# Performance work log

Measured on AMD Instinct MI355X. Metric: run time of the kernel, lower is better.

## Reference

```python
import jax, jax.numpy as jnp
import numpy as np

N_EMBD = 768
N_HEAD = 8
HEAD_DIM = N_EMBD // N_HEAD


def setup_inputs() -> dict:
    key = jax.random.key(0)
    k1, k2, k3 = jax.random.split(key, 3)
    B, T, C = 8, 1024, N_EMBD
    x = jax.random.normal(k1, (B, T, C), dtype=jnp.float32)
    # nn.Linear(C, 3C, bias=False): store as [C, 3C] so y = x @ W
    W_attn = jax.random.normal(k2, (C, 3 * C), dtype=jnp.float32) * (1.0 / np.sqrt(C))
    W_proj = jax.random.normal(k3, (C, C), dtype=jnp.float32) * (1.0 / np.sqrt(C))
    return {"x": x, "W_attn": W_attn, "W_proj": W_proj}


def reference(x, W_attn, W_proj):
    B, T, C = x.shape
    qkv = x @ W_attn                      # [B,T,3C]
    q, k, v = jnp.split(qkv, 3, axis=2)
    # [B,T,C] -> [B,H,T,D]
    def heads(t):
        return t.reshape(B, T, N_HEAD, HEAD_DIM).transpose(0, 2, 1, 3)
    q, k, v = heads(q), heads(k), heads(v)
    scale = 1.0 / np.sqrt(HEAD_DIM)
    att = jnp.einsum('bhtd,bhsd->bhts', q, k) * scale  # [B,H,T,T]
    causal = jnp.tril(jnp.ones((T, T), dtype=bool))
    att = jnp.where(causal[None, None], att, -jnp.inf)
    att = jax.nn.softmax(att, axis=-1)
    y = jnp.einsum('bhts,bhsd->bhtd', att, v)          # [B,H,T,D]
    y = y.transpose(0, 2, 1, 3).reshape(B, T, C)
    return y @ W_proj
```

## Files before the change

kernel.cpp:

```cpp
#include <hip/hip_runtime.h>
#include <stdint.h>

#define Bz 8
#define Tz 1024
#define Cz 768
#define Hz 8
#define Dz 96
#define BHz 64
#define Kz 768

typedef __bf16 bf16x8 __attribute__((ext_vector_type(8)));
typedef unsigned short u16x8 __attribute__((ext_vector_type(8)));
typedef float f32x4 __attribute__((ext_vector_type(4)));

__device__ __forceinline__ unsigned short f2bf(float f) {
  union { float f; unsigned int u; } v; v.f = f;
  unsigned int u = v.u;
  return (unsigned short)((u + 0x7fffu + ((u >> 16) & 1u)) >> 16);
}

__device__ __forceinline__ unsigned int cvtpk(float a, float b) {
  unsigned int r;
  asm("v_cvt_pk_bf16_f32 %0, %1, %2" : "=v"(r) : "v"(a), "v"(b));
  return r;
}

#if defined(__has_builtin)
#if __has_builtin(__builtin_amdgcn_exp2f)
#define EXP2(x) __builtin_amdgcn_exp2f(x)
#endif
#endif
#ifndef EXP2
#define EXP2(x) __expf((x) * 0.6931471805599453f)
#endif

typedef const __attribute__((address_space(1))) void* gas_ptr;
typedef __attribute__((address_space(3))) void* las_ptr;
__device__ __forceinline__ void gl16(const void* g, void* l) {
  __builtin_amdgcn_global_load_lds((gas_ptr)g, (las_ptr)l, 16, 0, 0);
}

__global__ __launch_bounds__(256) void cast_f32_bf16(const float* __restrict__ in,
                                                     unsigned short* __restrict__ out) {
  int i = (blockIdx.x * 256 + threadIdx.x) * 4;
  float4 v = *(const float4*)(in + i);
  union { unsigned short s[4]; uint2 u; } o;
  o.s[0] = f2bf(v.x); o.s[1] = f2bf(v.y); o.s[2] = f2bf(v.z); o.s[3] = f2bf(v.w);
  *(uint2*)(out + i) = o.u;
}

__global__ __launch_bounds__(256) void transpose_cast(const float* __restrict__ in,
                                                      unsigned short* __restrict__ out,
                                                      int R, int Cc) {
  __shared__ unsigned short t[64][72];
  int bx = blockIdx.x * 64;
  int by = blockIdx.y * 64;
  int tid = threadIdx.x;
#pragma unroll
  for (int i = 0; i < 16; i++) {
    int idx = tid + i * 256;
    int r = idx >> 6, c = idx & 63;
    t[c][r] = f2bf(in[(by + r) * Cc + bx + c]);
  }
  __syncthreads();
#pragma unroll
  for (int i = 0; i < 16; i++) {
    int idx = tid + i * 256;
    int r = idx >> 6, c = idx & 63;
    out[(bx + r) * R + by + c] = t[r][c];
  }
}

template <int MODE>
__global__ __launch_bounds__(256)
void gemm128(const unsigned short* __restrict__ A,
             const unsigned short* __restrict__ Bt,
             unsigned short* __restrict__ obf,
             float* __restrict__ of32) {
  __shared__ unsigned short Asm[128 * 32];
  __shared__ unsigned short Bsm[128 * 32];
  const int tid = threadIdx.x;
  const int wave = tid >> 6, lane = tid & 63;
  const int quad = lane >> 4, l16 = lane & 15;
  const int bm = blockIdx.x, bn = blockIdx.y;
  const int wm = (wave >> 1) * 64, wn = (wave & 1) * 64;

  f32x4 zero = {0.f, 0.f, 0.f, 0.f};
  f32x4 acc[4][4];
#pragma unroll
  for (int i = 0; i < 4; i++)
#pragma unroll
    for (int j = 0; j < 4; j++) acc[i][j] = zero;

  const int rr = lane >> 2, c8 = (lane & 3) * 8;
  const unsigned short* Ag0 = A + (size_t)(bm * 128 + wave * 32 + rr) * Kz + c8;
  const unsigned short* Ag1 = Ag0 + 16 * Kz;
  const unsigned short* Bg0 = Bt + (size_t)(bn * 128 + wave * 32 + rr) * Kz + c8;
  const unsigned short* Bg1 = Bg0 + 16 * Kz;
  unsigned short* lA0 = &Asm[wave * 1024];
  unsigned short* lA1 = lA0 + 512;
  unsigned short* lB0 = &Bsm[wave * 1024];
  unsigned short* lB1 = lB0 + 512;

  for (int k0 = 0; k0 < Kz; k0 += 32) {
    __syncthreads();
    gl16(Ag0 + k0, lA0);
    gl16(Ag1 + k0, lA1);
    gl16(Bg0 + k0, lB0);
    gl16(Bg1 + k0, lB1);
    __syncthreads();
    bf16x8 af[4], bfr[4];
#pragma unroll
    for (int mi = 0; mi < 4; mi++)
      af[mi] = *(const bf16x8*)&Asm[(wm + mi * 16 + l16) * 32 + quad * 8];
#pragma unroll
    for (int ni = 0; ni < 4; ni++)
      bfr[ni] = *(const bf16x8*)&Bsm[(wn + ni * 16 + l16) * 32 + quad * 8];
#pragma unroll
    for (int mi = 0; mi < 4; mi++)
#pragma unroll
      for (int ni = 0; ni < 4; ni++)
        acc[mi][ni] = __builtin_amdgcn_mfma_f32_16x16x32_bf16(af[mi], bfr[ni], acc[mi][ni], 0, 0, 0);
  }

#pragma unroll
  for (int mi = 0; mi < 4; mi++) {
    int row = bm * 128 + wm + mi * 16 + quad * 4;
    if (MODE == 0) {
      int b = row >> 10;
      int t = row & 1023;
#pragma unroll
      for (int ni = 0; ni < 4; ni++) {
        int col = bn * 128 + wn + ni * 16 + l16;
        int which = col / 768;
        int cc = col - which * 768;
        int h = cc / 96;
        int d = cc - h * 96;
        if (which == 2) {
          int base = ((2 * 64 + b * 8 + h) * 96 + d) * 1024 + t;
          union { unsigned short s[4]; uint2 u; } o;
#pragma unroll
          for (int r = 0; r < 4; r++) o.s[r] = f2bf(acc[mi][ni][r]);
          *(uint2*)(obf + base) = o.u;
        } else {
          int base = ((which * 64 + b * 8 + h) * 1024 + t) * 96 + d;
#pragma unroll
          for (int r = 0; r < 4; r++) obf[base + r * 96] = f2bf(acc[mi][ni][r]);
        }
      }
    } else {
#pragma unroll
      for (int ni = 0; ni < 4; ni++) {
        int col = bn * 128 + wn + ni * 16 + l16;
#pragma unroll
        for (int r = 0; r < 4; r++) of32[(row + r) * 768 + col] = acc[mi][ni][r];
      }
    }
  }
}

__global__ __launch_bounds__(256, 4)
void attn(const unsigned short* __restrict__ qkv, unsigned short* __restrict__ y) {
  const int bh = blockIdx.x;
  const int by = blockIdx.y;
  const int q0 = (15 - by) * 64;
  const int tid = threadIdx.x;
  const int wave = tid >> 6, lane = tid & 63;
  const int quad = lane >> 4, l16 = lane & 15;
  const int qw0 = q0 + wave * 16;
  const int b = bh >> 3, h = bh & 7;

  const unsigned short* Qh = qkv + bh * Tz * Dz;
  const unsigned short* Kh = qkv + (BHz + bh) * Tz * Dz;
  const unsigned short* Vt = qkv + 2 * BHz * Tz * Dz + bh * Dz * Tz;

  __shared__ unsigned short Vsm[96 * 128];

  bf16x8 aq[3];
#pragma unroll
  for (int kd = 0; kd < 3; kd++)
    aq[kd] = *(const bf16x8*)(Qh + (qw0 + l16) * Dz + kd * 32 + quad * 8);

  f32x4 zero = {0.f, 0.f, 0.f, 0.f};
  f32x4 acc_o[6];
#pragma unroll
  for (int i = 0; i < 6; i++) acc_o[i] = zero;
  const float NEG = -__builtin_inff();
  float mrow = NEG, lrow = 0.f;
  const float cs = 0.14724538519872735f;
  const int t_abs = qw0 + l16;

  const int vrow = wave * 24 + (lane >> 4);
  const int vch = lane & 15;

  const int s_last = (q0 >> 7) << 7;
  for (int s0 = 0; s0 <= s_last; s0 += 128) {
    __syncthreads();
#pragma unroll
    for (int g = 0; g < 6; g++) {
      const int row = vrow + g * 4;
      gl16(Vt + row * Tz + s0 + ((vch ^ (row & 7)) << 3),
           &Vsm[(wave * 24 + g * 4) * 128]);
    }

    const int srem = qw0 + 15 - s0;
    const int nlim = min(7, srem >> 4);
    const int klim = min(3, srem >> 5);

    f32x4 sacc[8];
#pragma unroll
    for (int ni = 0; ni < 8; ni++) {
      if (ni <= nlim) {
        sacc[ni] = zero;
#pragma unroll
        for (int kd = 0; kd < 3; kd++) {
          bf16x8 bk = *(const bf16x8*)(Kh + (s0 + ni * 16 + l16) * Dz + kd * 32 + quad * 8);
          sacc[ni] = __builtin_amdgcn_mfma_f32_16x16x32_bf16(bk, aq[kd], sacc[ni], 0, 0, 0);
        }
      }
    }

    float rmx[4] = {NEG, NEG, NEG, NEG};
#pragma unroll
    for (int ni = 0; ni < 8; ni++) {
      if (ni <= nlim) {
        if (s0 + ni * 16 + 15 > qw0) {
          const int s_base = s0 + ni * 16 + quad * 4;
#pragma unroll
          for (int r = 0; r < 4; r++)
            if (s_base + r > t_abs) sacc[ni][r] = NEG;
        }
#pragma unroll
        for (int r = 0; r < 4; r++) rmx[r] = fmaxf(rmx[r], sacc[ni][r]);
      }
    }
    float rmax = fmaxf(fmaxf(rmx[0], rmx[1]), fmaxf(rmx[2], rmx[3]));
    rmax = fmaxf(rmax, __shfl_xor(rmax, 16));
    rmax = fmaxf(rmax, __shfl_xor(rmax, 32));

    int ok = (rmax <= mrow + 54.0f) ? 1 : 0;
    if (!__all(ok)) {
      float mnew = fmaxf(mrow, rmax);
      float alpha = EXP2((mrow - mnew) * cs);
      mrow = mnew;
      lrow *= alpha;
      float av[4];
#pragma unroll
      for (int r = 0; r < 4; r++) av[r] = __shfl(alpha, quad * 4 + r);
#pragma unroll
      for (int di = 0; di < 6; di++)
#pragma unroll
        for (int r = 0; r < 4; r++) acc_o[di][r] *= av[r];
    }

    const float nmc = -mrow * cs;
    float rs[4] = {0.f, 0.f, 0.f, 0.f};
    unsigned int pk[8][2];
#pragma unroll
    for (int ni = 0; ni < 8; ni++) {
      if (ni <= nlim) {
        float p0 = EXP2(fmaf(sacc[ni][0], cs, nmc));
        float p1 = EXP2(fmaf(sacc[ni][1], cs, nmc));
        float p2 = EXP2(fmaf(sacc[ni][2], cs, nmc));
        float p3 = EXP2(fmaf(sacc[ni][3], cs, nmc));
        rs[0] += p0; rs[1] += p1; rs[2] += p2; rs[3] += p3;
        pk[ni][0] = cvtpk(p0, p1);
        pk[ni][1] = cvtpk(p2, p3);
      } else {
        pk[ni][0] = 0u; pk[ni][1] = 0u;
      }
    }
    lrow += (rs[0] + rs[1]) + (rs[2] + rs[3]);

    __syncthreads();

#pragma unroll
    for (int kc = 0; kc < 4; kc++) {
      if (kc <= klim) {
        const unsigned int a0 = pk[2 * kc][0], a1 = pk[2 * kc][1];
        const unsigned int b0 = pk[2 * kc + 1][0], b1 = pk[2 * kc + 1][1];
        const unsigned int s0w = (quad < 2) ? b0 : a0;
        const unsigned int s1w = (quad < 2) ? b1 : a1;
        const unsigned int u0 = (unsigned int)__shfl_xor((int)s0w, 32);
        const unsigned int u1 = (unsigned int)__shfl_xor((int)s1w, 32);
        const unsigned int t0w = (quad == 0 || quad == 3) ? u0 : ((quad == 1) ? a0 : b0);
        const unsigned int t1w = (quad == 0 || quad == 3) ? u1 : ((quad == 1) ? a1 : b1);
        const unsigned int r0 = (unsigned int)__shfl_xor((int)t0w, 16);
        const unsigned int r1 = (unsigned int)__shfl_xor((int)t1w, 16);
        union { unsigned int w[4]; bf16x8 v; } ap;
        ap.w[0] = (quad == 0) ? a0 : ((quad == 2) ? u0 : r0);
        ap.w[1] = (quad == 0) ? a1 : ((quad == 2) ? u1 : r1);
        ap.w[2] = (quad == 0) ? r0 : ((quad == 1) ? u0 : ((quad == 2) ? r0 : b0));
        ap.w[3] = (quad == 0) ? r1 : ((quad == 1) ? u1 : ((quad == 2) ? r1 : b1));
#pragma unroll
        for (int di = 0; di < 6; di++) {
          bf16x8 bv = *(const bf16x8*)&Vsm[(di * 16 + l16) * 128 +
                                           (((kc * 4 + quad) ^ (l16 & 7)) << 3)];
          acc_o[di] = __builtin_amdgcn_mfma_f32_16x16x32_bf16(ap.v, bv, acc_o[di], 0, 0, 0);
        }
      }
    }
  }

  lrow += __shfl_xor(lrow, 16);
  lrow += __shfl_xor(lrow, 32);
  float linv = 1.f / lrow;
  float lv[4];
#pragma unroll
  for (int r = 0; r < 4; r++) lv[r] = __shfl(linv, quad * 4 + r);
#pragma unroll
  for (int r = 0; r < 4; r++) {
    int t = qw0 + quad * 4 + r;
#pragma unroll
    for (int di = 0; di < 6; di++) {
      int d = di * 16 + l16;
      y[(b * Tz + t) * Cz + h * Dz + d] = f2bf(acc_o[di][r] * lv[r]);
    }
  }
}

#define OFF_XB   0u
#define OFF_WAT  12582912u
#define OFF_WPT  16121856u
#define OFF_QKV  17301504u
#define OFF_Y    55050240u

extern "C" void kernel_launch(void* const* d_in, const int* in_sizes, int n_in,
                              void* d_out, int out_size, void* d_ws, size_t ws_size,
                              hipStream_t stream) {
  const float* x  = (const float*)d_in[0];
  const float* Wa = (const float*)d_in[1];
  const float* Wp = (const float*)d_in[2];
  float* out = (float*)d_out;
  uint8_t* ws = (uint8_t*)d_ws;
  unsigned short* xb  = (unsigned short*)(ws + OFF_XB);
  unsigned short* Wat = (unsigned short*)(ws + OFF_WAT);
  unsigned short* Wpt = (unsigned short*)(ws + OFF_WPT);
  unsigned short* qkv = (unsigned short*)(ws + OFF_QKV);
  unsigned short* y   = (unsigned short*)(ws + OFF_Y);

  cast_f32_bf16<<<6144, 256, 0, stream>>>(x, xb);
  transpose_cast<<<dim3(36, 12), 256, 0, stream>>>(Wa, Wat, 768, 2304);
  transpose_cast<<<dim3(12, 12), 256, 0, stream>>>(Wp, Wpt, 768, 768);
  gemm128<0><<<dim3(64, 18), 256, 0, stream>>>(xb, Wat, qkv, nullptr);
  attn<<<dim3(64, 16), 256, 0, stream>>>(qkv, y);
  gemm128<1><<<dim3(64, 6), 256, 0, stream>>>(y, Wpt, nullptr, out);
}
```

Measured before the change: 205.3 us.

## Merge prep kernels and double GEMM K-tile with XOR-swizzled LDS layout

The three cast/transpose launches become a single prep kernel that picks its job from the block index, which removes two kernel launches. The GEMM K-step grows from 32 to 64, halving the number of barrier pairs per tile. LDS chunks are now stored with an XOR swizzle on row, which is meant to avoid bank conflicts in the fragment reads. LDS use per block doubles.

```diff
diff --git a/kernel.cpp b/kernel.cpp
--- a/kernel.cpp
+++ b/kernel.cpp
@@ -40,22 +40,26 @@
   __builtin_amdgcn_global_load_lds((gas_ptr)g, (las_ptr)l, 16, 0, 0);
 }
 
-__global__ __launch_bounds__(256) void cast_f32_bf16(const float* __restrict__ in,
-                                                     unsigned short* __restrict__ out) {
-  int i = (blockIdx.x * 256 + threadIdx.x) * 4;
-  float4 v = *(const float4*)(in + i);
-  union { unsigned short s[4]; uint2 u; } o;
-  o.s[0] = f2bf(v.x); o.s[1] = f2bf(v.y); o.s[2] = f2bf(v.z); o.s[3] = f2bf(v.w);
-  *(uint2*)(out + i) = o.u;
-}
-
-__global__ __launch_bounds__(256) void transpose_cast(const float* __restrict__ in,
-                                                      unsigned short* __restrict__ out,
-                                                      int R, int Cc) {
+__global__ __launch_bounds__(256) void prep(const float* __restrict__ x,
+                                            unsigned short* __restrict__ xb,
+                                            const float* __restrict__ Wa,
+                                            unsigned short* __restrict__ Wat,
+                                            const float* __restrict__ Wp,
+                                            unsigned short* __restrict__ Wpt) {
   __shared__ unsigned short t[64][72];
-  int bx = blockIdx.x * 64;
-  int by = blockIdx.y * 64;
-  int tid = threadIdx.x;
+  const int bid = blockIdx.x;
+  const int tid = threadIdx.x;
+  if (bid < 6144) {
+    int i = (bid * 256 + tid) * 4;
+    float4 v = *(const float4*)(x + i);
+    union { unsigned short s[4]; uint2 u; } o;
+    o.s[0] = f2bf(v.x); o.s[1] = f2bf(v.y); o.s[2] = f2bf(v.z); o.s[3] = f2bf(v.w);
+    *(uint2*)(xb + i) = o.u;
+    return;
+  }
+  const float* in; unsigned short* out; int R, Cc, bx, by;
+  if (bid < 6576) { int q = bid - 6144; in = Wa; out = Wat; R = 768; Cc = 2304; bx = (q % 36) * 64; by = (q / 36) * 64; }
+  else            { int q = bid - 6576; in = Wp; out = Wpt; R = 768; Cc = 768;  bx = (q % 12) * 64; by = (q / 12) * 64; }
 #pragma unroll
   for (int i = 0; i < 16; i++) {
     int idx = tid + i * 256;
@@ -77,8 +81,8 @@
              const unsigned short* __restrict__ Bt,
              unsigned short* __restrict__ obf,
              float* __restrict__ of32) {
-  __shared__ unsigned short Asm[128 * 32];
-  __shared__ unsigned short Bsm[128 * 32];
+  __shared__ unsigned short Asm[128 * 64];
+  __shared__ unsigned short Bsm[128 * 64];
   const int tid = threadIdx.x;
   const int wave = tid >> 6, lane = tid & 63;
   const int quad = lane >> 4, l16 = lane & 15;
@@ -92,35 +96,40 @@
 #pragma unroll
     for (int j = 0; j < 4; j++) acc[i][j] = zero;
 
-  const int rr = lane >> 2, c8 = (lane & 3) * 8;
-  const unsigned short* Ag0 = A + (size_t)(bm * 128 + wave * 32 + rr) * Kz + c8;
-  const unsigned short* Ag1 = Ag0 + 16 * Kz;
-  const unsigned short* Bg0 = Bt + (size_t)(bn * 128 + wave * 32 + rr) * Kz + c8;
-  const unsigned short* Bg1 = Bg0 + 16 * Kz;
-  unsigned short* lA0 = &Asm[wave * 1024];
-  unsigned short* lA1 = lA0 + 512;
-  unsigned short* lB0 = &Bsm[wave * 1024];
-  unsigned short* lB1 = lB0 + 512;
-
-  for (int k0 = 0; k0 < Kz; k0 += 32) {
+  const int srow = lane >> 3;
+  const int sch = (lane & 7) ^ srow;
+  const unsigned short* Ag[4];
+  const unsigned short* Bg[4];
+#pragma unroll
+  for (int g = 0; g < 4; g++) {
+    Ag[g] = A + (size_t)(bm * 128 + g * 32 + wave * 8 + srow) * Kz + sch * 8;
+    Bg[g] = Bt + (size_t)(bn * 128 + g * 32 + wave * 8 + srow) * Kz + sch * 8;
+  }
+
+  for (int k0 = 0; k0 < Kz; k0 += 64) {
     __syncthreads();
-    gl16(Ag0 + k0, lA0);
-    gl16(Ag1 + k0, lA1);
-    gl16(Bg0 + k0, lB0);
-    gl16(Bg1 + k0, lB1);
+#pragma unroll
+    for (int g = 0; g < 4; g++) {
+      gl16(Ag[g] + k0, &Asm[(g * 32 + wave * 8) * 64]);
+      gl16(Bg[g] + k0, &Bsm[(g * 32 + wave * 8) * 64]);
+    }
     __syncthreads();
-    bf16x8 af[4], bfr[4];
-#pragma unroll
-    for (int mi = 0; mi < 4; mi++)
-      af[mi] = *(const bf16x8*)&Asm[(wm + mi * 16 + l16) * 32 + quad * 8];
-#pragma unroll
-    for (int ni = 0; ni < 4; ni++)
-      bfr[ni] = *(const bf16x8*)&Bsm[(wn + ni * 16 + l16) * 32 + quad * 8];
-#pragma unroll
-    for (int mi = 0; mi < 4; mi++)
+#pragma unroll
+    for (int kk = 0; kk < 2; kk++) {
+      const int rc = (((kk * 4 + quad) ^ (l16 & 7)) << 3);
+      bf16x8 af[4], bfr[4];
+#pragma unroll
+      for (int mi = 0; mi < 4; mi++)
+        af[mi] = *(const bf16x8*)&Asm[(wm + mi * 16 + l16) * 64 + rc];
 #pragma unroll
       for (int ni = 0; ni < 4; ni++)
-        acc[mi][ni] = __builtin_amdgcn_mfma_f32_16x16x32_bf16(af[mi], bfr[ni], acc[mi][ni], 0, 0, 0);
+        bfr[ni] = *(const bf16x8*)&Bsm[(wn + ni * 16 + l16) * 64 + rc];
+#pragma unroll
+      for (int mi = 0; mi < 4; mi++)
+#pragma unroll
+        for (int ni = 0; ni < 4; ni++)
+          acc[mi][ni] = __builtin_amdgcn_mfma_f32_16x16x32_bf16(af[mi], bfr[ni], acc[mi][ni], 0, 0, 0);
+    }
   }
 
 #pragma unroll
@@ -339,9 +348,7 @@
   unsigned short* qkv = (unsigned short*)(ws + OFF_QKV);
   unsigned short* y   = (unsigned short*)(ws + OFF_Y);
 
-  cast_f32_bf16<<<6144, 256, 0, stream>>>(x, xb);
-  transpose_cast<<<dim3(36, 12), 256, 0, stream>>>(Wa, Wat, 768, 2304);
-  transpose_cast<<<dim3(12, 12), 256, 0, stream>>>(Wp, Wpt, 768, 768);
+  prep<<<6720, 256, 0, stream>>>(x, xb, Wa, Wat, Wp, Wpt);
   gemm128<0><<<dim3(64, 18), 256, 0, stream>>>(xb, Wat, qkv, nullptr);
   attn<<<dim3(64, 16), 256, 0, stream>>>(qkv, y);
   gemm128<1><<<dim3(64, 6), 256, 0, stream>>>(y, Wpt, nullptr, out);
```

Measured after the change: 200.6 us. 1.02x faster.
